# Kernel optimization log

Hardware: AMD Instinct MI355X
Metric: run time of the kernel (lower is better)

Reference implementation:

```python
import jax, jax.numpy as jnp
import numpy as np

N_NODES = 100000
N_LAYERS = 3


def spmm(rows, cols, vals, x):
    # sparse [N,N] @ dense [N,d] via gather + segment_sum
    msg = vals[:, None] * x[cols]  # [E, d]
    return jax.ops.segment_sum(msg, rows, num_segments=N_NODES)


def setup_inputs() -> dict:
    key = jax.random.key(0)
    k1, k2, k3, k4, k5, k6, k7 = jax.random.split(key, 7)
    E, D, B = 1600000, 64, 4096
    return {
        "embeds": jax.random.normal(k1, (N_NODES, D), dtype=jnp.float32),
        "adj_rows": jax.random.randint(k2, (E,), 0, N_NODES, dtype=jnp.int32),
        "adj_cols": jax.random.randint(k3, (E,), 0, N_NODES, dtype=jnp.int32),
        "adj_vals": jax.random.uniform(k4, (E,), dtype=jnp.float32),
        "node": jax.random.randint(k5, (B,), 0, N_NODES, dtype=jnp.int32),
        "pos_node": jax.random.randint(k6, (B,), 0, N_NODES, dtype=jnp.int32),
        "neg_node": jax.random.randint(k7, (B,), 0, N_NODES, dtype=jnp.int32),
    }


def reference(embeds, adj_rows, adj_cols, adj_vals, node, pos_node, neg_node):
    # GraphConv: multi-hop propagation with running accumulation (mean pooling fused)
    agg = embeds
    acc = embeds  # running sum of layer embeddings (hop 0)
    for _ in range(N_LAYERS):
        agg = spmm(adj_rows, adj_cols, adj_vals, agg)
        acc = acc + agg
    pooled = acc / (N_LAYERS + 1)  # aggr == 'mean'
    return (
        pooled[node],
        pooled[pos_node],
        pooled[neg_node],
        embeds[node],
        embeds[pos_node],
        embeds[neg_node],
    )
```

## Files before the change

### kernel.cpp

```cpp
#include <hip/hip_runtime.h>


#define NBUCKET 3125
#define BSHIFT  5
#define BMASK   31
#define NCHUNK  256

static __device__ __forceinline__ ushort f2bf(float f) {
    unsigned u = __float_as_uint(f);
    unsigned r = (u + 0x7fffu + ((u >> 16) & 1u)) >> 16;
    return (ushort)r;
}
static __device__ __forceinline__ float bf2f(ushort b) {
    return __uint_as_float(((unsigned)b) << 16);
}

__global__ __launch_bounds__(256) void f2bf_k(
    const float* __restrict__ in, ushort* __restrict__ out, int n4)
{
    int i = blockIdx.x * blockDim.x + threadIdx.x;
    if (i >= n4) return;
    float4 v = *(const float4*)(in + (long)i * 4);
    ushort4 o;
    o.x = f2bf(v.x); o.y = f2bf(v.y); o.z = f2bf(v.z); o.w = f2bf(v.w);
    *(ushort4*)(out + (long)i * 4) = o;
}

__global__ __launch_bounds__(1024) void count_k(
    const int* __restrict__ rows, int* __restrict__ cnt, int E, int chunkE)
{
    __shared__ unsigned h[NBUCKET];
    int c = blockIdx.x;
    for (int b = threadIdx.x; b < NBUCKET; b += 1024) h[b] = 0u;
    __syncthreads();
    int s = c * chunkE;
    int e = min(s + chunkE, E);
    for (int j = s + (int)threadIdx.x; j < e; j += 1024)
        atomicAdd(&h[rows[j] >> BSHIFT], 1u);
    __syncthreads();
    int* o = cnt + (long)c * NBUCKET;
    for (int b = threadIdx.x; b < NBUCKET; b += 1024) o[b] = (int)h[b];
}

__global__ __launch_bounds__(256) void localscan_k(
    const int* __restrict__ cnt, int* __restrict__ offs,
    int* __restrict__ totals)
{
    int b = blockIdx.x * 256 + threadIdx.x;
    if (b >= NBUCKET) return;
    int run = 0;
    #pragma unroll 8
    for (int c = 0; c < NCHUNK; ++c) {
        long i = (long)c * NBUCKET + b;
        int v = cnt[i];
        offs[i] = run;
        run += v;
    }
    totals[b] = run;
}

__global__ __launch_bounds__(1024) void scan_fused_k(
    const int* __restrict__ totals, int* __restrict__ bucket_start, int nbucket)
{
    __shared__ int sm[1024];
    __shared__ int carry_s;
    if (threadIdx.x == 0) carry_s = 0;
    __syncthreads();
    int ntile = (nbucket + 1023) / 1024;
    for (int t = 0; t < ntile; ++t) {
        int i = t * 1024 + threadIdx.x;
        int v = (i < nbucket) ? totals[i] : 0;
        sm[threadIdx.x] = v;
        __syncthreads();
        for (int off = 1; off < 1024; off <<= 1) {
            int add = (threadIdx.x >= off) ? sm[threadIdx.x - off] : 0;
            __syncthreads();
            sm[threadIdx.x] += add;
            __syncthreads();
        }
        int c0 = carry_s;
        if (i < nbucket) bucket_start[i] = c0 + sm[threadIdx.x] - v;
        __syncthreads();
        if (threadIdx.x == 1023) carry_s = c0 + sm[1023];
        __syncthreads();
    }
    if (threadIdx.x == 0) bucket_start[nbucket] = carry_s;
}

__global__ __launch_bounds__(1024) void scatter3_k(
    const int* __restrict__ rows, const int* __restrict__ cols,
    const float* __restrict__ vals, const int* __restrict__ offs,
    const int* __restrict__ bucket_start,
    int2* __restrict__ edges, int E, int chunkE)
{
    __shared__ int cur[NBUCKET];
    int c = blockIdx.x;
    const int* o = offs + (long)c * NBUCKET;
    for (int b = threadIdx.x; b < NBUCKET; b += 1024)
        cur[b] = o[b] + bucket_start[b];
    __syncthreads();
    int s = c * chunkE;
    int e = min(s + chunkE, E);
    for (int j = s + (int)threadIdx.x; j < e; j += 1024) {
        int r = rows[j];
        int pos = atomicAdd(&cur[r >> BSHIFT], 1);
        edges[pos] = make_int2(((r & BMASK) << 17) | cols[j],
                               __float_as_int(vals[j]));
    }
}

__global__ __launch_bounds__(256) void sort_bkt_k(
    const int* __restrict__ bucket_start, const int2* __restrict__ edges_in,
    int2* __restrict__ edges_out, int* __restrict__ row_start, int nbucket)
{
    __shared__ int cur[4][32];
    int w = (int)(threadIdx.x >> 6);
    int lane = (int)(threadIdx.x & 63);
    int bk = blockIdx.x * 4 + w;
    if (bk >= nbucket) return;
    int s = bucket_start[bk];
    int e = bucket_start[bk + 1];
    if (lane < 32) cur[w][lane] = 0;
    for (int j = s + lane; j < e; j += 64)
        atomicAdd(&cur[w][(unsigned)edges_in[j].x >> 17], 1);
    if (lane == 0) {
        int run = s;
        #pragma unroll
        for (int r = 0; r < 32; ++r) {
            int c = cur[w][r];
            cur[w][r] = run;
            row_start[bk * 32 + r] = run;
            run += c;
        }
    }
    for (int j = s + lane; j < e; j += 64) {
        int2 ed = edges_in[j];
        int pos = atomicAdd(&cur[w][(unsigned)ed.x >> 17], 1);
        edges_out[pos] = ed;
    }
    if (bk == nbucket - 1 && lane == 0) row_start[nbucket * 32] = e;
}

#define GMA(k) float p##k = __int_as_float(ee##k.y) * \
    bf2f(x[(long)(ee##k.x & 0x1FFFF) * 64 + d])

__global__ __launch_bounds__(256) void spmm_csr_k(
    const int* __restrict__ row_start, const int2* __restrict__ edges,
    const ushort* __restrict__ x, ushort* __restrict__ y, int N)
{
    int wid = __builtin_amdgcn_readfirstlane((int)(threadIdx.x >> 6));
    int r = blockIdx.x * 4 + wid;
    if (r >= N) return;
    int d = (int)(threadIdx.x & 63);
    int s = row_start[r];
    int e = row_start[r + 1];
    float a0 = 0.f, a1 = 0.f, a2 = 0.f, a3 = 0.f;
    float a4 = 0.f, a5 = 0.f, a6 = 0.f, a7 = 0.f;
    float a8 = 0.f, a9 = 0.f, a10 = 0.f, a11 = 0.f;
    float a12 = 0.f, a13 = 0.f, a14 = 0.f, a15 = 0.f;
    int j = s;
    for (; j + 16 <= e; j += 16) {
        int2 ee0  = edges[j];      int2 ee1  = edges[j + 1];
        int2 ee2  = edges[j + 2];  int2 ee3  = edges[j + 3];
        int2 ee4  = edges[j + 4];  int2 ee5  = edges[j + 5];
        int2 ee6  = edges[j + 6];  int2 ee7  = edges[j + 7];
        int2 ee8  = edges[j + 8];  int2 ee9  = edges[j + 9];
        int2 ee10 = edges[j + 10]; int2 ee11 = edges[j + 11];
        int2 ee12 = edges[j + 12]; int2 ee13 = edges[j + 13];
        int2 ee14 = edges[j + 14]; int2 ee15 = edges[j + 15];
        GMA(0); GMA(1); GMA(2); GMA(3); GMA(4); GMA(5); GMA(6); GMA(7);
        GMA(8); GMA(9); GMA(10); GMA(11); GMA(12); GMA(13); GMA(14); GMA(15);
        a0 += p0;  a1 += p1;  a2 += p2;  a3 += p3;
        a4 += p4;  a5 += p5;  a6 += p6;  a7 += p7;
        a8 += p8;  a9 += p9;  a10 += p10; a11 += p11;
        a12 += p12; a13 += p13; a14 += p14; a15 += p15;
    }
    for (; j + 8 <= e; j += 8) {
        int2 ee0 = edges[j];     int2 ee1 = edges[j + 1];
        int2 ee2 = edges[j + 2]; int2 ee3 = edges[j + 3];
        int2 ee4 = edges[j + 4]; int2 ee5 = edges[j + 5];
        int2 ee6 = edges[j + 6]; int2 ee7 = edges[j + 7];
        GMA(0); GMA(1); GMA(2); GMA(3); GMA(4); GMA(5); GMA(6); GMA(7);
        a0 += p0; a1 += p1; a2 += p2; a3 += p3;
        a4 += p4; a5 += p5; a6 += p6; a7 += p7;
    }
    for (; j + 4 <= e; j += 4) {
        int2 ee0 = edges[j];     int2 ee1 = edges[j + 1];
        int2 ee2 = edges[j + 2]; int2 ee3 = edges[j + 3];
        GMA(0); GMA(1); GMA(2); GMA(3);
        a0 += p0; a1 += p1; a2 += p2; a3 += p3;
    }
    for (; j < e; ++j) {
        int2 ee0 = edges[j];
        GMA(0);
        a0 += p0;
    }
    float sum = (((a0 + a1) + (a2 + a3)) + ((a4 + a5) + (a6 + a7)))
              + (((a8 + a9) + (a10 + a11)) + ((a12 + a13) + (a14 + a15)));
    y[(long)r * 64 + d] = f2bf(sum);
}

__global__ __launch_bounds__(256) void init_out_k(
    const float* __restrict__ emb, const int* __restrict__ n0,
    const int* __restrict__ n1, const int* __restrict__ n2,
    float* __restrict__ out, int B)
{
    int tid = blockIdx.x * blockDim.x + threadIdx.x;
    int total = 3 * B * 16;
    if (tid >= total) return;
    int arr = tid / (B * 16);
    int rem = tid - arr * (B * 16);
    int b = rem >> 4;
    int d4 = rem & 15;
    const int* __restrict__ idx = (arr == 0) ? n0 : ((arr == 1) ? n1 : n2);
    float4 v = *(const float4*)(emb + (long)idx[b] * 64 + d4 * 4);
    float4 q = make_float4(0.25f * v.x, 0.25f * v.y, 0.25f * v.z, 0.25f * v.w);
    *(float4*)(out + (long)arr * B * 64 + (long)rem * 4) = q;
    *(float4*)(out + (long)(arr + 3) * B * 64 + (long)rem * 4) = v;
}

__global__ __launch_bounds__(256) void gather_add_k(
    const ushort* __restrict__ agg, const int* __restrict__ n0,
    const int* __restrict__ n1, const int* __restrict__ n2,
    float* __restrict__ out, int B)
{
    int tid = blockIdx.x * blockDim.x + threadIdx.x;
    int total = 3 * B * 16;
    if (tid >= total) return;
    int arr = tid / (B * 16);
    int rem = tid - arr * (B * 16);
    int b = rem >> 4;
    int d4 = rem & 15;
    const int* __restrict__ idx = (arr == 0) ? n0 : ((arr == 1) ? n1 : n2);
    ushort4 v = *(const ushort4*)(agg + (long)idx[b] * 64 + d4 * 4);
    float* o = out + (long)arr * B * 64 + (long)rem * 4;
    float4 cur = *(float4*)o;
    cur.x += 0.25f * bf2f(v.x); cur.y += 0.25f * bf2f(v.y);
    cur.z += 0.25f * bf2f(v.z); cur.w += 0.25f * bf2f(v.w);
    *(float4*)o = cur;
}

extern "C" void kernel_launch(void* const* d_in, const int* in_sizes, int n_in,
                              void* d_out, int out_size, void* d_ws, size_t ws_size,
                              hipStream_t stream)
{
    const float* emb  = (const float*)d_in[0];
    const int*   rows = (const int*)d_in[1];
    const int*   cols = (const int*)d_in[2];
    const float* vals = (const float*)d_in[3];
    const int*   node = (const int*)d_in[4];
    const int*   pos  = (const int*)d_in[5];
    const int*   neg  = (const int*)d_in[6];
    float* out = (float*)d_out;

    const int E = in_sizes[1];
    const int B = in_sizes[4];
    const int N = in_sizes[0] / 64;
    const size_t nd = (size_t)N * 64;
    const int chunkE = (E + NCHUNK - 1) / NCHUNK;
    const int nbucket = (N + BMASK) >> BSHIFT;

    ushort* aggA        = (ushort*)d_ws;
    ushort* aggB        = aggA + nd;
    int2*  edges        = (int2*)(aggB + nd);
    int2*  edges2       = edges + E;
    int*   cnt          = (int*)(edges2 + E);
    int*   totals       = cnt + (long)NCHUNK * NBUCKET;
    int*   bucket_start = totals + NBUCKET;
    int*   row_start    = bucket_start + NBUCKET + 1;
    int*   offs         = (int*)edges2;

    const int gtotal   = 3 * B * 16;
    const int gblocks  = (gtotal + 255) / 256;
    const int cblocks  = ((int)(nd / 4) + 255) / 256;
    const int bblocks  = (nbucket + 255) / 256;
    const int dblocks  = (nbucket + 3) / 4;
    const int rblocks  = (N + 3) / 4;

    init_out_k<<<gblocks, 256, 0, stream>>>(emb, node, pos, neg, out, B);
    f2bf_k<<<cblocks, 256, 0, stream>>>(emb, aggB, (int)(nd / 4));

    count_k<<<NCHUNK, 1024, 0, stream>>>(rows, cnt, E, chunkE);
    localscan_k<<<bblocks, 256, 0, stream>>>(cnt, offs, totals);
    scan_fused_k<<<1, 1024, 0, stream>>>(totals, bucket_start, nbucket);
    scatter3_k<<<NCHUNK, 1024, 0, stream>>>(rows, cols, vals, offs, bucket_start, edges, E, chunkE);
    sort_bkt_k<<<dblocks, 256, 0, stream>>>(bucket_start, edges, edges2, row_start, nbucket);

    spmm_csr_k<<<rblocks, 256, 0, stream>>>(row_start, edges2, aggB, aggA, N);
    gather_add_k<<<gblocks, 256, 0, stream>>>(aggA, node, pos, neg, out, B);

    spmm_csr_k<<<rblocks, 256, 0, stream>>>(row_start, edges2, aggA, aggB, N);
    gather_add_k<<<gblocks, 256, 0, stream>>>(aggB, node, pos, neg, out, B);

    spmm_csr_k<<<rblocks, 256, 0, stream>>>(row_start, edges2, aggB, aggA, N);
    gather_add_k<<<gblocks, 256, 0, stream>>>(aggA, node, pos, neg, out, B);
}
```

Baseline: 203.7 us.

## Use block-per-bucket sort and masked single-loop SpMM with padded edge tail

The bucket sort now assigns one 256-thread block per bucket instead of one wavefront per bucket, adding syncthreads between its phases. The SpMM kernel drops its 8/4/1-edge remainder loops and handles every row with a single 16-wide loop whose out-of-range edges are masked to zero weight. The edge array is padded with 16 zero entries so the over-read at the end stays in bounds. This removes serialized tail iterations but issues extra wasted gathers for rows whose edge count is not a multiple of 16.

```diff
diff --git a/kernel.cpp b/kernel.cpp
--- a/kernel.cpp
+++ b/kernel.cpp
@@ -113,35 +113,40 @@
     const int* __restrict__ bucket_start, const int2* __restrict__ edges_in,
     int2* __restrict__ edges_out, int* __restrict__ row_start, int nbucket)
 {
-    __shared__ int cur[4][32];
-    int w = (int)(threadIdx.x >> 6);
-    int lane = (int)(threadIdx.x & 63);
-    int bk = blockIdx.x * 4 + w;
-    if (bk >= nbucket) return;
+    __shared__ int cnt_s[32];
+    __shared__ int cur_s[32];
+    int bk = blockIdx.x;
+    int t = (int)threadIdx.x;
     int s = bucket_start[bk];
     int e = bucket_start[bk + 1];
-    if (lane < 32) cur[w][lane] = 0;
-    for (int j = s + lane; j < e; j += 64)
-        atomicAdd(&cur[w][(unsigned)edges_in[j].x >> 17], 1);
-    if (lane == 0) {
+    if (t < 32) cnt_s[t] = 0;
+    __syncthreads();
+    for (int j = s + t; j < e; j += 256)
+        atomicAdd(&cnt_s[(unsigned)edges_in[j].x >> 17], 1);
+    __syncthreads();
+    if (t == 0) {
         int run = s;
         #pragma unroll
         for (int r = 0; r < 32; ++r) {
-            int c = cur[w][r];
-            cur[w][r] = run;
+            int c = cnt_s[r];
+            cur_s[r] = run;
             row_start[bk * 32 + r] = run;
             run += c;
         }
     }
-    for (int j = s + lane; j < e; j += 64) {
+    __syncthreads();
+    for (int j = s + t; j < e; j += 256) {
         int2 ed = edges_in[j];
-        int pos = atomicAdd(&cur[w][(unsigned)ed.x >> 17], 1);
+        int pos = atomicAdd(&cur_s[(unsigned)ed.x >> 17], 1);
         edges_out[pos] = ed;
     }
-    if (bk == nbucket - 1 && lane == 0) row_start[nbucket * 32] = e;
-}
-
-#define GMA(k) float p##k = __int_as_float(ee##k.y) * \
+    if (bk == nbucket - 1) {
+        if (t == 0) row_start[nbucket * 32] = e;
+        if (t < 16) edges_out[e + t] = make_int2(0, 0);
+    }
+}
+
+#define GMAM(k) float p##k = ((j + k) < e ? __int_as_float(ee##k.y) : 0.f) * \
     bf2f(x[(long)(ee##k.x & 0x1FFFF) * 64 + d])
 
 __global__ __launch_bounds__(256) void spmm_csr_k(
@@ -158,8 +163,7 @@
     float a4 = 0.f, a5 = 0.f, a6 = 0.f, a7 = 0.f;
     float a8 = 0.f, a9 = 0.f, a10 = 0.f, a11 = 0.f;
     float a12 = 0.f, a13 = 0.f, a14 = 0.f, a15 = 0.f;
-    int j = s;
-    for (; j + 16 <= e; j += 16) {
+    for (int j = s; j < e; j += 16) {
         int2 ee0  = edges[j];      int2 ee1  = edges[j + 1];
         int2 ee2  = edges[j + 2];  int2 ee3  = edges[j + 3];
         int2 ee4  = edges[j + 4];  int2 ee5  = edges[j + 5];
@@ -168,32 +172,14 @@
         int2 ee10 = edges[j + 10]; int2 ee11 = edges[j + 11];
         int2 ee12 = edges[j + 12]; int2 ee13 = edges[j + 13];
         int2 ee14 = edges[j + 14]; int2 ee15 = edges[j + 15];
-        GMA(0); GMA(1); GMA(2); GMA(3); GMA(4); GMA(5); GMA(6); GMA(7);
-        GMA(8); GMA(9); GMA(10); GMA(11); GMA(12); GMA(13); GMA(14); GMA(15);
+        GMAM(0); GMAM(1); GMAM(2); GMAM(3);
+        GMAM(4); GMAM(5); GMAM(6); GMAM(7);
+        GMAM(8); GMAM(9); GMAM(10); GMAM(11);
+        GMAM(12); GMAM(13); GMAM(14); GMAM(15);
         a0 += p0;  a1 += p1;  a2 += p2;  a3 += p3;
         a4 += p4;  a5 += p5;  a6 += p6;  a7 += p7;
         a8 += p8;  a9 += p9;  a10 += p10; a11 += p11;
         a12 += p12; a13 += p13; a14 += p14; a15 += p15;
-    }
-    for (; j + 8 <= e; j += 8) {
-        int2 ee0 = edges[j];     int2 ee1 = edges[j + 1];
-        int2 ee2 = edges[j + 2]; int2 ee3 = edges[j + 3];
-        int2 ee4 = edges[j + 4]; int2 ee5 = edges[j + 5];
-        int2 ee6 = edges[j + 6]; int2 ee7 = edges[j + 7];
-        GMA(0); GMA(1); GMA(2); GMA(3); GMA(4); GMA(5); GMA(6); GMA(7);
-        a0 += p0; a1 += p1; a2 += p2; a3 += p3;
-        a4 += p4; a5 += p5; a6 += p6; a7 += p7;
-    }
-    for (; j + 4 <= e; j += 4) {
-        int2 ee0 = edges[j];     int2 ee1 = edges[j + 1];
-        int2 ee2 = edges[j + 2]; int2 ee3 = edges[j + 3];
-        GMA(0); GMA(1); GMA(2); GMA(3);
-        a0 += p0; a1 += p1; a2 += p2; a3 += p3;
-    }
-    for (; j < e; ++j) {
-        int2 ee0 = edges[j];
-        GMA(0);
-        a0 += p0;
     }
     float sum = (((a0 + a1) + (a2 + a3)) + ((a4 + a5) + (a6 + a7)))
               + (((a8 + a9) + (a10 + a11)) + ((a12 + a13) + (a14 + a15)));
@@ -264,7 +250,7 @@
     ushort* aggB        = aggA + nd;
     int2*  edges        = (int2*)(aggB + nd);
     int2*  edges2       = edges + E;
-    int*   cnt          = (int*)(edges2 + E);
+    int*   cnt          = (int*)(edges2 + E + 16);
     int*   totals       = cnt + (long)NCHUNK * NBUCKET;
     int*   bucket_start = totals + NBUCKET;
     int*   row_start    = bucket_start + NBUCKET + 1;
@@ -274,7 +260,6 @@
     const int gblocks  = (gtotal + 255) / 256;
     const int cblocks  = ((int)(nd / 4) + 255) / 256;
     const int bblocks  = (nbucket + 255) / 256;
-    const int dblocks  = (nbucket + 3) / 4;
     const int rblocks  = (N + 3) / 4;
 
     init_out_k<<<gblocks, 256, 0, stream>>>(emb, node, pos, neg, out, B);
@@ -284,7 +269,7 @@
     localscan_k<<<bblocks, 256, 0, stream>>>(cnt, offs, totals);
     scan_fused_k<<<1, 1024, 0, stream>>>(totals, bucket_start, nbucket);
     scatter3_k<<<NCHUNK, 1024, 0, stream>>>(rows, cols, vals, offs, bucket_start, edges, E, chunkE);
-    sort_bkt_k<<<dblocks, 256, 0, stream>>>(bucket_start, edges, edges2, row_start, nbucket);
+    sort_bkt_k<<<nbucket, 256, 0, stream>>>(bucket_start, edges, edges2, row_start, nbucket);
 
     spmm_csr_k<<<rblocks, 256, 0, stream>>>(row_start, edges2, aggB, aggA, N);
     gather_add_k<<<gblocks, 256, 0, stream>>>(aggA, node, pos, neg, out, B);
```

Result: slower. 236.3 us (+16.0%).
